# Performance work log

Hardware: AMD Instinct MI355X
Metric: run time of the kernel (lower is better)

## Reference

```python
import jax, jax.numpy as jnp
import numpy as np

N_NODES = 50000
BN_EPS = 1e-5


def sage_conv(x, src, dst, Wl, Wr, b):
    # mean-aggregate neighbor features: message from src -> dst
    msg = x[src]                                             # [E, Din]
    s = jax.ops.segment_sum(msg, dst, num_segments=N_NODES)  # [N, Din]
    cnt = jax.ops.segment_sum(jnp.ones((src.shape[0],), x.dtype), dst,
                              num_segments=N_NODES)          # [N]
    mean = s / jnp.maximum(cnt, 1.0)[:, None]
    # PyG SAGEConv: lin_l(aggregated) (+bias) + lin_r(self), root_weight=True
    return mean @ Wl + b + x @ Wr


def batch_norm(x, gamma, beta):
    mu = jnp.mean(x, axis=0)
    var = jnp.var(x, axis=0)
    return (x - mu) * jax.lax.rsqrt(var + BN_EPS) * gamma + beta


def setup_inputs() -> dict:
    key = jax.random.key(0)
    ks = jax.random.split(key, 16)
    D_IN, D_H, D_OUT = 128, 128, 64
    x = jax.random.normal(ks[0], (N_NODES, D_IN), dtype=jnp.float32)
    edge_index = jax.random.randint(ks[1], (2, 800000), 0, N_NODES, dtype=jnp.int32)

    def xavier(k, din, dout):
        lim = float(np.sqrt(6.0 / (din + dout)))
        return jax.random.uniform(k, (din, dout), jnp.float32, -lim, lim)

    return {
        "x": x, "edge_index": edge_index,
        "Wl0": xavier(ks[2], D_IN, D_H), "Wr0": xavier(ks[3], D_IN, D_H),
        "b0": jnp.zeros((D_H,), jnp.float32),
        "g0": jnp.ones((D_H,), jnp.float32), "be0": jnp.zeros((D_H,), jnp.float32),
        "Wl1": xavier(ks[4], D_H, D_H), "Wr1": xavier(ks[5], D_H, D_H),
        "b1": jnp.zeros((D_H,), jnp.float32),
        "g1": jnp.ones((D_H,), jnp.float32), "be1": jnp.zeros((D_H,), jnp.float32),
        "Wl2": xavier(ks[6], D_H, D_OUT), "Wr2": xavier(ks[7], D_H, D_OUT),
        "b2": jnp.zeros((D_OUT,), jnp.float32),
    }


def reference(x, edge_index, Wl0, Wr0, b0, g0, be0,
              Wl1, Wr1, b1, g1, be1, Wl2, Wr2, b2):
    src, dst = edge_index[0], edge_index[1]
    h = sage_conv(x, src, dst, Wl0, Wr0, b0)
    h = jax.nn.relu(batch_norm(h, g0, be0))
    h = sage_conv(h, src, dst, Wl1, Wr1, b1)
    h = jax.nn.relu(batch_norm(h, g1, be1))
    h = sage_conv(h, src, dst, Wl2, Wr2, b2)
    return jax.nn.log_softmax(h, axis=-1)
```

## Files before the change

kernel.cpp:

```cpp
#include <hip/hip_runtime.h>
#include <hip/hip_bf16.h>

#define D_IN 128
#define D_OUT 64
#define BN_EPS 1e-5f
#define NB_PART 512

typedef short short8 __attribute__((ext_vector_type(8)));
typedef float f32x4 __attribute__((ext_vector_type(4)));
typedef float f32x2 __attribute__((ext_vector_type(2)));
typedef unsigned short ushort_t;
typedef unsigned int uint_t;

__device__ __forceinline__ float bf16lo(uint_t v) { return __uint_as_float(v << 16); }
__device__ __forceinline__ float bf16hi(uint_t v) { return __uint_as_float(v & 0xffff0000u); }
__device__ __forceinline__ ushort_t f2bf(float f) {
    union { __hip_bfloat16 h; ushort_t u; } cv;
    cv.h = __float2bfloat16(f);
    return cv.u;
}
__device__ __forceinline__ f32x4 ntload4(const float* p) {
    return __builtin_nontemporal_load((const f32x4*)p);
}


__global__ void hist_kernel(const int* __restrict__ dst, int* __restrict__ cnt, int E) {
    int i = blockIdx.x * 256 + threadIdx.x;
    if (i < E) atomicAdd(&cnt[__builtin_nontemporal_load(&dst[i])], 1);
}

__global__ void scan_part_kernel(const int* __restrict__ cnt, int* __restrict__ bsum, int n) {
    int i = blockIdx.x * 256 + threadIdx.x;
    int v = (i < n) ? cnt[i] : 0;
#pragma unroll
    for (int off = 1; off < 64; off <<= 1) v += __shfl_xor(v, off);
    __shared__ int ws[4];
    int lane = threadIdx.x & 63, wid = threadIdx.x >> 6;
    if (lane == 0) ws[wid] = v;
    __syncthreads();
    if (threadIdx.x == 0) bsum[blockIdx.x] = ws[0] + ws[1] + ws[2] + ws[3];
}

__global__ void scan_mid_kernel(const int* __restrict__ bsum, int* __restrict__ bpre,
                                int* __restrict__ offs, int PB, int n) {
    int t = threadIdx.x;
    int v = (t < PB) ? bsum[t] : 0;
    int lane = t & 63, wid = t >> 6;
    int sc = v;
#pragma unroll
    for (int off = 1; off < 64; off <<= 1) {
        int u = __shfl_up(sc, off);
        if (lane >= off) sc += u;
    }
    __shared__ int ws[4];
    if (lane == 63) ws[wid] = sc;
    __syncthreads();
    int wb = 0;
    for (int w = 0; w < 4; w++) if (w < wid) wb += ws[w];
    int incl = sc + wb;
    if (t < PB) bpre[t] = incl - v;
    if (t == PB - 1) offs[n] = incl;
}

__global__ void scan_final_kernel(const int* __restrict__ cnt, const int* __restrict__ bpre,
                                  int* __restrict__ offs, int* __restrict__ cursor, int n) {
    int b = blockIdx.x, t = threadIdx.x;
    int i = b * 256 + t;
    int v = (i < n) ? cnt[i] : 0;
    int lane = t & 63, wid = t >> 6;
    int sc = v;
#pragma unroll
    for (int off = 1; off < 64; off <<= 1) {
        int u = __shfl_up(sc, off);
        if (lane >= off) sc += u;
    }
    __shared__ int ws[4];
    if (lane == 63) ws[wid] = sc;
    __syncthreads();
    int wb = 0;
    for (int w = 0; w < 4; w++) if (w < wid) wb += ws[w];
    if (i < n) {
        int e = bpre[b] + wb + sc - v;
        offs[i] = e;
        cursor[i] = e;
    }
}

__global__ void scatter_kernel(const int* __restrict__ src, const int* __restrict__ dst,
                               int* __restrict__ cursor, ushort_t* __restrict__ sorted_src,
                               int E, int passW) {
    int lo = blockIdx.y * passW, hi = lo + passW;
    int i = blockIdx.x * 256 + threadIdx.x;
    if (i < E) {
        int d = __builtin_nontemporal_load(&dst[i]);
        if (d >= lo && d < hi) {
            int s = __builtin_nontemporal_load(&src[i]);
            int p = atomicAdd(&cursor[d], 1);
            sorted_src[p] = (ushort_t)s;
        }
    }
}


__global__ void wswz_kernel(const float* __restrict__ Wl0, const float* __restrict__ Wr0,
                            const float* __restrict__ Wl1, const float* __restrict__ Wr1,
                            const float* __restrict__ Wl2, const float* __restrict__ Wr2,
                            short* __restrict__ o0l, short* __restrict__ o0r,
                            short* __restrict__ o1l, short* __restrict__ o1r,
                            short* __restrict__ o2l, short* __restrict__ o2r) {
    int layer = blockIdx.z;
    int Nn = (layer == 2) ? 64 : 128;
    const float* W;
    short* out;
    if (layer == 0) { W = blockIdx.y ? Wr0 : Wl0; out = blockIdx.y ? o0r : o0l; }
    else if (layer == 1) { W = blockIdx.y ? Wr1 : Wl1; out = blockIdx.y ? o1r : o1l; }
    else { W = blockIdx.y ? Wr2 : Wl2; out = blockIdx.y ? o2r : o2l; }
    int g = blockIdx.x * 256 + threadIdx.x;
    int nchunks = (Nn / 16) * 4;
    int chunk = g >> 6, lane = g & 63;
    if (chunk >= nchunks) return;
    int nf = chunk >> 2, kk = chunk & 3;
    short8 s;
#pragma unroll
    for (int j = 0; j < 8; j++) {
        float v = W[(size_t)(kk * 32 + (lane >> 4) * 8 + j) * Nn + nf * 16 + (lane & 15)];
        s[j] = (short)f2bf(v);
    }
    *(short8*)&out[((size_t)(chunk << 6) + lane) * 8] = s;
}


template <int TN, bool BN>
__global__ __launch_bounds__(TN == 128 ? 256 : 128)
void gemm2_mfma(const float* __restrict__ A, const short* __restrict__ WlF,
                const short* __restrict__ WrF, ushort_t* __restrict__ Yb,
                float* __restrict__ Z, const float* __restrict__ stats,
                const float* __restrict__ gamma, const float* __restrict__ beta, int M) {
    __shared__ short As[64 * 136];
    __shared__ float sc[128], sh[128];
    const int tid = threadIdx.x;
    const int lane = tid & 63;
    const int w = tid >> 6;
    const int row0 = blockIdx.x * 64;
    const int NT = (TN == 128) ? 256 : 128;

    if (BN) {
        if (tid < 128) {
            float invM = 1.0f / (float)M;
            float mu = stats[tid] * invM;
            float var = stats[128 + tid] * invM - mu * mu;
            float scale = gamma[tid] * rsqrtf(var + BN_EPS);
            sc[tid] = scale;
            sh[tid] = beta[tid] - mu * scale;
        }
        __syncthreads();
    }

    for (int c = tid; c < 1024; c += NT) {
        int r = c >> 4, off = (c & 15) * 8;
        short8 v8 = {0, 0, 0, 0, 0, 0, 0, 0};
        if (row0 + r < M) {
            const float* ap = &A[(size_t)(row0 + r) * 128 + off];
            f32x4 f0 = ntload4(ap);
            f32x4 f1 = ntload4(ap + 4);
            if (BN) {
#pragma unroll
                for (int j = 0; j < 4; j++) {
                    f0[j] = fmaxf(f0[j] * sc[off + j] + sh[off + j], 0.f);
                    f1[j] = fmaxf(f1[j] * sc[off + 4 + j] + sh[off + 4 + j], 0.f);
                }
            }
#pragma unroll
            for (int j = 0; j < 4; j++) {
                v8[j] = (short)f2bf(f0[j]);
                v8[4 + j] = (short)f2bf(f1[j]);
            }
        }
        *(short8*)&As[r * 136 + off] = v8;
    }
    __syncthreads();

    const short* WF;
    bool isY;
    int col0;
    if (TN == 128) {
        isY = (w < 2);
        WF = isY ? WlF : WrF;
        col0 = (w & 1) * 64;
    } else {
        isY = (w == 0);
        WF = isY ? WlF : WrF;
        col0 = 0;
    }

    short8 a[4][4];
#pragma unroll
    for (int m = 0; m < 4; m++)
#pragma unroll
        for (int kk = 0; kk < 4; kk++)
            a[m][kk] = *(const short8*)&As[(m * 16 + (lane & 15)) * 136 + kk * 32 + (lane >> 4) * 8];

    f32x4 acc[4][4];
#pragma unroll
    for (int m = 0; m < 4; m++)
#pragma unroll
        for (int n = 0; n < 4; n++) acc[m][n] = (f32x4){0.f, 0.f, 0.f, 0.f};

#pragma unroll
    for (int kk = 0; kk < 4; kk++) {
#pragma unroll
        for (int n = 0; n < 4; n++) {
            short8 b = *(const short8*)&WF[(size_t)(((col0 >> 4) + n) * 4 + kk) * 512 + lane * 8];
#pragma unroll
            for (int m = 0; m < 4; m++)
                acc[m][n] = __builtin_amdgcn_mfma_f32_16x16x32_bf16(a[m][kk], b, acc[m][n], 0, 0, 0);
        }
    }

#pragma unroll
    for (int m = 0; m < 4; m++) {
#pragma unroll
        for (int i = 0; i < 4; i++) {
            int gr = row0 + m * 16 + (lane >> 4) * 4 + i;
            if (gr < M) {
                if (isY) {
#pragma unroll
                    for (int n = 0; n < 4; n++)
                        Yb[(size_t)gr * TN + col0 + n * 16 + (lane & 15)] = f2bf(acc[m][n][i]);
                } else {
#pragma unroll
                    for (int n = 0; n < 4; n++)
                        Z[(size_t)gr * TN + col0 + n * 16 + (lane & 15)] = acc[m][n][i];
                }
            }
        }
    }
}


__global__ __launch_bounds__(256) void agg128_kernel(const ushort_t* __restrict__ Yb,
                                                     const int* __restrict__ offs,
                                                     const ushort_t* __restrict__ sorted_src,
                                                     const float* __restrict__ bias,
                                                     float* __restrict__ H, int N) {
    int node = blockIdx.x * 4 + (threadIdx.x >> 6);
    int lane = threadIdx.x & 63;
    if (node >= N) return;
    int s0 = offs[node], s1 = offs[node + 1];
    float a0 = 0.f, a1 = 0.f;
    int k = s0;
    for (; k + 8 <= s1; k += 8) {
        int idx[8];
#pragma unroll
        for (int j = 0; j < 8; j++) idx[j] = __builtin_nontemporal_load(&sorted_src[k + j]);
        uint_t v[8];
#pragma unroll
        for (int j = 0; j < 8; j++) v[j] = *(const uint_t*)&Yb[(size_t)idx[j] * 128 + lane * 2];
#pragma unroll
        for (int j = 0; j < 8; j++) {
            a0 += bf16lo(v[j]);
            a1 += bf16hi(v[j]);
        }
    }
    if (k + 4 <= s1) {
        int idx[4];
#pragma unroll
        for (int j = 0; j < 4; j++) idx[j] = __builtin_nontemporal_load(&sorted_src[k + j]);
#pragma unroll
        for (int j = 0; j < 4; j++) {
            uint_t v = *(const uint_t*)&Yb[(size_t)idx[j] * 128 + lane * 2];
            a0 += bf16lo(v);
            a1 += bf16hi(v);
        }
        k += 4;
    }
    for (; k < s1; k++) {
        uint_t v = *(const uint_t*)&Yb[(size_t)sorted_src[k] * 128 + lane * 2];
        a0 += bf16lo(v);
        a1 += bf16hi(v);
    }
    float inv = 1.0f / fmaxf((float)(s1 - s0), 1.0f);
    float2 b = *(const float2*)&bias[lane * 2];
    f32x2* hp = (f32x2*)&H[(size_t)node * 128 + lane * 2];
    f32x2 h = __builtin_nontemporal_load(hp);
    h[0] += a0 * inv + b.x;
    h[1] += a1 * inv + b.y;
    __builtin_nontemporal_store(h, hp);
}


__global__ __launch_bounds__(256) void agg_lsm_kernel(const ushort_t* __restrict__ Yb,
                                                      const int* __restrict__ offs,
                                                      const ushort_t* __restrict__ sorted_src,
                                                      const float* __restrict__ bias,
                                                      const float* __restrict__ Z,
                                                      float* __restrict__ out, int N) {
    int wv = blockIdx.x * 4 + (threadIdx.x >> 6);
    int lane = threadIdx.x & 63;
    int half = lane >> 5, l = lane & 31;
    int node = wv * 2 + half;
    if (node >= N) return;
    int s0 = offs[node], s1 = offs[node + 1];
    float a0 = 0.f, a1 = 0.f;
    int k = s0;
    for (; k + 4 <= s1; k += 4) {
        int idx[4];
#pragma unroll
        for (int j = 0; j < 4; j++) idx[j] = __builtin_nontemporal_load(&sorted_src[k + j]);
#pragma unroll
        for (int j = 0; j < 4; j++) {
            uint_t v = *(const uint_t*)&Yb[(size_t)idx[j] * 64 + l * 2];
            a0 += bf16lo(v);
            a1 += bf16hi(v);
        }
    }
    for (; k < s1; k++) {
        uint_t v = *(const uint_t*)&Yb[(size_t)sorted_src[k] * 64 + l * 2];
        a0 += bf16lo(v);
        a1 += bf16hi(v);
    }
    float inv = 1.0f / fmaxf((float)(s1 - s0), 1.0f);
    f32x2 zb = __builtin_nontemporal_load((const f32x2*)&Z[(size_t)node * 64 + l * 2]);
    float2 bb = *(const float2*)&bias[l * 2];
    float v0 = zb[0] + a0 * inv + bb.x;
    float v1 = zb[1] + a1 * inv + bb.y;
    float m = fmaxf(v0, v1);
#pragma unroll
    for (int off = 16; off; off >>= 1) m = fmaxf(m, __shfl_xor(m, off));
    float s = expf(v0 - m) + expf(v1 - m);
#pragma unroll
    for (int off = 16; off; off >>= 1) s += __shfl_xor(s, off);
    float ls = logf(s);
    f32x2 o;
    o[0] = v0 - m - ls;
    o[1] = v1 - m - ls;
    __builtin_nontemporal_store(o, (f32x2*)&out[(size_t)node * 64 + l * 2]);
}


__global__ __launch_bounds__(256) void bn_part_kernel(const float* __restrict__ H,
                                                      float* __restrict__ P, int M) {
    int b = blockIdx.x;
    int R = (M + NB_PART - 1) / NB_PART;
    int r0 = b * R, r1 = min(r0 + R, M);
    int colg = (threadIdx.x & 31) * 4;
    int rowoff = threadIdx.x >> 5;
    f32x4 s = {0.f, 0.f, 0.f, 0.f}, s2 = {0.f, 0.f, 0.f, 0.f};
    for (int r = r0 + rowoff; r < r1; r += 8) {
        f32x4 v = ntload4(&H[(size_t)r * 128 + colg]);
        s += v;
        s2 += v * v;
    }
    __shared__ float ls[256][8];
#pragma unroll
    for (int j = 0; j < 4; j++) {
        ls[threadIdx.x][j] = s[j];
        ls[threadIdx.x][4 + j] = s2[j];
    }
    __syncthreads();
    if (threadIdx.x < 32) {
#pragma unroll
        for (int j = 0; j < 8; j++) {
            float a = 0.f;
#pragma unroll
            for (int k = 0; k < 8; k++) a += ls[threadIdx.x + 32 * k][j];
            if (j < 4) P[(size_t)b * 256 + threadIdx.x * 4 + j] = a;
            else P[(size_t)b * 256 + 128 + threadIdx.x * 4 + (j - 4)] = a;
        }
    }
}

__global__ __launch_bounds__(1024) void bn_reduce_kernel(const float* __restrict__ P,
                                                         float* __restrict__ stats) {
    int c = threadIdx.x & 255, q = threadIdx.x >> 8;
    float acc = 0.f;
#pragma unroll 8
    for (int i = q * (NB_PART / 4); i < (q + 1) * (NB_PART / 4); i++)
        acc += P[(size_t)i * 256 + c];
    __shared__ float ls[4][256];
    ls[q][c] = acc;
    __syncthreads();
    if (threadIdx.x < 256) stats[c] = ls[0][c] + ls[1][c] + ls[2][c] + ls[3][c];
}


extern "C" void kernel_launch(void* const* d_in, const int* in_sizes, int n_in,
                              void* d_out, int out_size, void* d_ws, size_t ws_size,
                              hipStream_t stream) {
    const float* x   = (const float*)d_in[0];
    const int*   ei  = (const int*)d_in[1];
    const float* Wl0 = (const float*)d_in[2];
    const float* Wr0 = (const float*)d_in[3];
    const float* b0  = (const float*)d_in[4];
    const float* g0  = (const float*)d_in[5];
    const float* be0 = (const float*)d_in[6];
    const float* Wl1 = (const float*)d_in[7];
    const float* Wr1 = (const float*)d_in[8];
    const float* b1  = (const float*)d_in[9];
    const float* g1  = (const float*)d_in[10];
    const float* be1 = (const float*)d_in[11];
    const float* Wl2 = (const float*)d_in[12];
    const float* Wr2 = (const float*)d_in[13];
    const float* b2  = (const float*)d_in[14];

    const int N = in_sizes[0] / D_IN;
    const int E = in_sizes[1] / 2;
    const int PB = (N + 255) / 256;

    float* H = (float*)d_ws;
    float* Z2 = H + (size_t)N * D_IN;
    ushort_t* Yb = (ushort_t*)(Z2 + (size_t)N * D_OUT);
    int* cnt    = (int*)(Yb + (size_t)N * D_IN);
    int* offs   = cnt + N;
    int* cursor = offs + N + 1;
    int* bsum   = cursor + N;
    int* bpre   = bsum + 256;
    ushort_t* sorted = (ushort_t*)(bpre + 256);
    float* stats = (float*)(sorted + E + (E & 1));
    float* P = stats + 512;
    short* WlF0 = (short*)(P + NB_PART * 256);
    short* WrF0 = WlF0 + 16384;
    short* WlF1 = WrF0 + 16384;
    short* WrF1 = WlF1 + 16384;
    short* WlF2 = WrF1 + 16384;
    short* WrF2 = WlF2 + 8192;

    const int eb = (E + 255) / 256;

    hipMemsetAsync(cnt, 0, (size_t)N * sizeof(int), stream);
    hist_kernel<<<eb, 256, 0, stream>>>(ei + E, cnt, E);
    scan_part_kernel<<<PB, 256, 0, stream>>>(cnt, bsum, N);
    scan_mid_kernel<<<1, 256, 0, stream>>>(bsum, bpre, offs, PB, N);
    scan_final_kernel<<<PB, 256, 0, stream>>>(cnt, bpre, offs, cursor, N);
    scatter_kernel<<<dim3(eb, 2), 256, 0, stream>>>(ei, ei + E, cursor, sorted, E, (N + 1) / 2);

    wswz_kernel<<<dim3(8, 2, 3), 256, 0, stream>>>(Wl0, Wr0, Wl1, Wr1, Wl2, Wr2,
                                                   WlF0, WrF0, WlF1, WrF1, WlF2, WrF2);

    const int gb = (N + 63) / 64;
    const int ab = (N + 3) / 4;
    const int ab2 = (N + 7) / 8;

    gemm2_mfma<128, false><<<gb, 256, 0, stream>>>(x, WlF0, WrF0, Yb, H,
                                                   nullptr, nullptr, nullptr, N);
    agg128_kernel<<<ab, 256, 0, stream>>>(Yb, offs, sorted, b0, H, N);
    bn_part_kernel<<<NB_PART, 256, 0, stream>>>(H, P, N);
    bn_reduce_kernel<<<1, 1024, 0, stream>>>(P, stats);

    gemm2_mfma<128, true><<<gb, 256, 0, stream>>>(H, WlF1, WrF1, Yb, H,
                                                  stats, g0, be0, N);
    agg128_kernel<<<ab, 256, 0, stream>>>(Yb, offs, sorted, b1, H, N);
    bn_part_kernel<<<NB_PART, 256, 0, stream>>>(H, P, N);
    bn_reduce_kernel<<<1, 1024, 0, stream>>>(P, stats + 256);

    gemm2_mfma<64, true><<<gb, 128, 0, stream>>>(H, WlF2, WrF2, Yb, Z2,
                                                 stats + 256, g1, be1, N);
    agg_lsm_kernel<<<ab2, 256, 0, stream>>>(Yb, offs, sorted, b2, Z2, (float*)d_out, N);
}
```

Before: 372.8 us.

## Store hidden activations and root-term outputs in bf16 instead of fp32

Converts the intermediate H (post-aggregation hidden) and Z (self-term GEMM output) buffers from fp32 to bf16 across the GEMM, aggregation, batch-norm statistics and log-softmax kernels. This roughly halves the memory traffic of the bandwidth-bound intermediate writes and reads. The aggregation kernel is reworked to process two nodes per wavefront with 4 columns per lane, and the BN partial reduction now reads 8 bf16 values per thread. The cost is extra rounding error in the hidden activations and in the BN statistics computed from them.

```diff
diff --git a/kernel.cpp b/kernel.cpp
--- a/kernel.cpp
+++ b/kernel.cpp
@@ -9,11 +9,14 @@
 typedef short short8 __attribute__((ext_vector_type(8)));
 typedef float f32x4 __attribute__((ext_vector_type(4)));
 typedef float f32x2 __attribute__((ext_vector_type(2)));
+typedef unsigned int u32x4 __attribute__((ext_vector_type(4)));
+typedef unsigned int u32x2 __attribute__((ext_vector_type(2)));
 typedef unsigned short ushort_t;
 typedef unsigned int uint_t;
 
 __device__ __forceinline__ float bf16lo(uint_t v) { return __uint_as_float(v << 16); }
 __device__ __forceinline__ float bf16hi(uint_t v) { return __uint_as_float(v & 0xffff0000u); }
+__device__ __forceinline__ float bf2f(ushort_t u) { return __uint_as_float(((uint_t)u) << 16); }
 __device__ __forceinline__ ushort_t f2bf(float f) {
     union { __hip_bfloat16 h; ushort_t u; } cv;
     cv.h = __float2bfloat16(f);
@@ -130,11 +133,11 @@
 }
 
 
-template <int TN, bool BN>
+template <int TN, bool BF16IN>
 __global__ __launch_bounds__(TN == 128 ? 256 : 128)
-void gemm2_mfma(const float* __restrict__ A, const short* __restrict__ WlF,
+void gemm2_mfma(const void* __restrict__ Ain, const short* __restrict__ WlF,
                 const short* __restrict__ WrF, ushort_t* __restrict__ Yb,
-                float* __restrict__ Z, const float* __restrict__ stats,
+                ushort_t* __restrict__ Zb, const float* __restrict__ stats,
                 const float* __restrict__ gamma, const float* __restrict__ beta, int M) {
     __shared__ short As[64 * 136];
     __shared__ float sc[128], sh[128];
@@ -144,7 +147,7 @@
     const int row0 = blockIdx.x * 64;
     const int NT = (TN == 128) ? 256 : 128;
 
-    if (BN) {
+    if (BF16IN) {
         if (tid < 128) {
             float invM = 1.0f / (float)M;
             float mu = stats[tid] * invM;
@@ -160,36 +163,42 @@
         int r = c >> 4, off = (c & 15) * 8;
         short8 v8 = {0, 0, 0, 0, 0, 0, 0, 0};
         if (row0 + r < M) {
-            const float* ap = &A[(size_t)(row0 + r) * 128 + off];
-            f32x4 f0 = ntload4(ap);
-            f32x4 f1 = ntload4(ap + 4);
-            if (BN) {
+            if (BF16IN) {
+                const ushort_t* ap = (const ushort_t*)Ain + (size_t)(row0 + r) * 128 + off;
+                short8 h = *(const short8*)ap;
+#pragma unroll
+                for (int j = 0; j < 8; j++) {
+                    float f = bf2f((ushort_t)h[j]);
+                    f = fmaxf(f * sc[off + j] + sh[off + j], 0.f);
+                    v8[j] = (short)f2bf(f);
+                }
+            } else {
+                const float* ap = (const float*)Ain + (size_t)(row0 + r) * 128 + off;
+                f32x4 f0 = ntload4(ap);
+                f32x4 f1 = ntload4(ap + 4);
 #pragma unroll
                 for (int j = 0; j < 4; j++) {
-                    f0[j] = fmaxf(f0[j] * sc[off + j] + sh[off + j], 0.f);
-                    f1[j] = fmaxf(f1[j] * sc[off + 4 + j] + sh[off + 4 + j], 0.f);
+                    v8[j] = (short)f2bf(f0[j]);
+                    v8[4 + j] = (short)f2bf(f1[j]);
                 }
             }
-#pragma unroll
-            for (int j = 0; j < 4; j++) {
-                v8[j] = (short)f2bf(f0[j]);
-                v8[4 + j] = (short)f2bf(f1[j]);
-            }
         }
         *(short8*)&As[r * 136 + off] = v8;
     }
     __syncthreads();
 
     const short* WF;
-    bool isY;
+    ushort_t* D;
     int col0;
     if (TN == 128) {
-        isY = (w < 2);
+        bool isY = (w < 2);
         WF = isY ? WlF : WrF;
+        D = isY ? Yb : Zb;
         col0 = (w & 1) * 64;
     } else {
-        isY = (w == 0);
+        bool isY = (w == 0);
         WF = isY ? WlF : WrF;
+        D = isY ? Yb : Zb;
         col0 = 0;
     }
 
@@ -223,15 +232,9 @@
         for (int i = 0; i < 4; i++) {
             int gr = row0 + m * 16 + (lane >> 4) * 4 + i;
             if (gr < M) {
-                if (isY) {
-#pragma unroll
-                    for (int n = 0; n < 4; n++)
-                        Yb[(size_t)gr * TN + col0 + n * 16 + (lane & 15)] = f2bf(acc[m][n][i]);
-                } else {
-#pragma unroll
-                    for (int n = 0; n < 4; n++)
-                        Z[(size_t)gr * TN + col0 + n * 16 + (lane & 15)] = acc[m][n][i];
-                }
+#pragma unroll
+                for (int n = 0; n < 4; n++)
+                    D[(size_t)gr * TN + col0 + n * 16 + (lane & 15)] = f2bf(acc[m][n][i]);
             }
         }
     }
@@ -242,24 +245,29 @@
                                                      const int* __restrict__ offs,
                                                      const ushort_t* __restrict__ sorted_src,
                                                      const float* __restrict__ bias,
-                                                     float* __restrict__ H, int N) {
-    int node = blockIdx.x * 4 + (threadIdx.x >> 6);
+                                                     const ushort_t* __restrict__ Zb,
+                                                     ushort_t* __restrict__ Hb, int N) {
+    int wv = blockIdx.x * 4 + (threadIdx.x >> 6);
     int lane = threadIdx.x & 63;
+    int half = lane >> 5, l = lane & 31;
+    int node = wv * 2 + half;
     if (node >= N) return;
     int s0 = offs[node], s1 = offs[node + 1];
-    float a0 = 0.f, a1 = 0.f;
+    float a0 = 0.f, a1 = 0.f, a2 = 0.f, a3 = 0.f;
     int k = s0;
     for (; k + 8 <= s1; k += 8) {
         int idx[8];
 #pragma unroll
         for (int j = 0; j < 8; j++) idx[j] = __builtin_nontemporal_load(&sorted_src[k + j]);
-        uint_t v[8];
-#pragma unroll
-        for (int j = 0; j < 8; j++) v[j] = *(const uint_t*)&Yb[(size_t)idx[j] * 128 + lane * 2];
+        u32x2 v[8];
+#pragma unroll
+        for (int j = 0; j < 8; j++) v[j] = *(const u32x2*)&Yb[(size_t)idx[j] * 128 + l * 4];
 #pragma unroll
         for (int j = 0; j < 8; j++) {
-            a0 += bf16lo(v[j]);
-            a1 += bf16hi(v[j]);
+            a0 += bf16lo(v[j][0]);
+            a1 += bf16hi(v[j][0]);
+            a2 += bf16lo(v[j][1]);
+            a3 += bf16hi(v[j][1]);
         }
     }
     if (k + 4 <= s1) {
@@ -268,24 +276,32 @@
         for (int j = 0; j < 4; j++) idx[j] = __builtin_nontemporal_load(&sorted_src[k + j]);
 #pragma unroll
         for (int j = 0; j < 4; j++) {
-            uint_t v = *(const uint_t*)&Yb[(size_t)idx[j] * 128 + lane * 2];
-            a0 += bf16lo(v);
-            a1 += bf16hi(v);
+            u32x2 v = *(const u32x2*)&Yb[(size_t)idx[j] * 128 + l * 4];
+            a0 += bf16lo(v[0]);
+            a1 += bf16hi(v[0]);
+            a2 += bf16lo(v[1]);
+            a3 += bf16hi(v[1]);
         }
         k += 4;
     }
     for (; k < s1; k++) {
-        uint_t v = *(const uint_t*)&Yb[(size_t)sorted_src[k] * 128 + lane * 2];
-        a0 += bf16lo(v);
-        a1 += bf16hi(v);
+        u32x2 v = *(const u32x2*)&Yb[(size_t)sorted_src[k] * 128 + l * 4];
+        a0 += bf16lo(v[0]);
+        a1 += bf16hi(v[0]);
+        a2 += bf16lo(v[1]);
+        a3 += bf16hi(v[1]);
     }
     float inv = 1.0f / fmaxf((float)(s1 - s0), 1.0f);
-    float2 b = *(const float2*)&bias[lane * 2];
-    f32x2* hp = (f32x2*)&H[(size_t)node * 128 + lane * 2];
-    f32x2 h = __builtin_nontemporal_load(hp);
-    h[0] += a0 * inv + b.x;
-    h[1] += a1 * inv + b.y;
-    __builtin_nontemporal_store(h, hp);
+    float4 bb = *(const float4*)&bias[l * 4];
+    u32x2 z = __builtin_nontemporal_load((const u32x2*)&Zb[(size_t)node * 128 + l * 4]);
+    float h0 = bf16lo(z[0]) + a0 * inv + bb.x;
+    float h1 = bf16hi(z[0]) + a1 * inv + bb.y;
+    float h2 = bf16lo(z[1]) + a2 * inv + bb.z;
+    float h3 = bf16hi(z[1]) + a3 * inv + bb.w;
+    u32x2 o;
+    o[0] = (uint_t)f2bf(h0) | ((uint_t)f2bf(h1) << 16);
+    o[1] = (uint_t)f2bf(h2) | ((uint_t)f2bf(h3) << 16);
+    __builtin_nontemporal_store(o, (u32x2*)&Hb[(size_t)node * 128 + l * 4]);
 }
 
 
@@ -293,7 +309,7 @@
                                                       const int* __restrict__ offs,
                                                       const ushort_t* __restrict__ sorted_src,
                                                       const float* __restrict__ bias,
-                                                      const float* __restrict__ Z,
+                                                      const ushort_t* __restrict__ Zb,
                                                       float* __restrict__ out, int N) {
     int wv = blockIdx.x * 4 + (threadIdx.x >> 6);
     int lane = threadIdx.x & 63;
@@ -320,10 +336,10 @@
         a1 += bf16hi(v);
     }
     float inv = 1.0f / fmaxf((float)(s1 - s0), 1.0f);
-    f32x2 zb = __builtin_nontemporal_load((const f32x2*)&Z[(size_t)node * 64 + l * 2]);
+    uint_t z = *(const uint_t*)&Zb[(size_t)node * 64 + l * 2];
     float2 bb = *(const float2*)&bias[l * 2];
-    float v0 = zb[0] + a0 * inv + bb.x;
-    float v1 = zb[1] + a1 * inv + bb.y;
+    float v0 = bf16lo(z) + a0 * inv + bb.x;
+    float v1 = bf16hi(z) + a1 * inv + bb.y;
     float m = fmaxf(v0, v1);
 #pragma unroll
     for (int off = 16; off; off >>= 1) m = fmaxf(m, __shfl_xor(m, off));
@@ -338,35 +354,46 @@
 }
 
 
-__global__ __launch_bounds__(256) void bn_part_kernel(const float* __restrict__ H,
+__global__ __launch_bounds__(256) void bn_part_kernel(const ushort_t* __restrict__ Hb,
                                                       float* __restrict__ P, int M) {
     int b = blockIdx.x;
     int R = (M + NB_PART - 1) / NB_PART;
     int r0 = b * R, r1 = min(r0 + R, M);
-    int colg = (threadIdx.x & 31) * 4;
-    int rowoff = threadIdx.x >> 5;
-    f32x4 s = {0.f, 0.f, 0.f, 0.f}, s2 = {0.f, 0.f, 0.f, 0.f};
-    for (int r = r0 + rowoff; r < r1; r += 8) {
-        f32x4 v = ntload4(&H[(size_t)r * 128 + colg]);
-        s += v;
-        s2 += v * v;
-    }
-    __shared__ float ls[256][8];
-#pragma unroll
-    for (int j = 0; j < 4; j++) {
+    int colg = (threadIdx.x & 15) * 8;
+    int rowoff = threadIdx.x >> 4;
+    float s[8], s2[8];
+#pragma unroll
+    for (int j = 0; j < 8; j++) { s[j] = 0.f; s2[j] = 0.f; }
+    for (int r = r0 + rowoff; r < r1; r += 16) {
+        u32x4 v = __builtin_nontemporal_load((const u32x4*)&Hb[(size_t)r * 128 + colg]);
+#pragma unroll
+        for (int q = 0; q < 4; q++) {
+            float flo = bf16lo(v[q]);
+            float fhi = bf16hi(v[q]);
+            s[2 * q] += flo;
+            s2[2 * q] += flo * flo;
+            s[2 * q + 1] += fhi;
+            s2[2 * q + 1] += fhi * fhi;
+        }
+    }
+    __shared__ float ls[256][16];
+#pragma unroll
+    for (int j = 0; j < 8; j++) {
         ls[threadIdx.x][j] = s[j];
-        ls[threadIdx.x][4 + j] = s2[j];
-    }
-    __syncthreads();
-    if (threadIdx.x < 32) {
-#pragma unroll
-        for (int j = 0; j < 8; j++) {
-            float a = 0.f;
-#pragma unroll
-            for (int k = 0; k < 8; k++) a += ls[threadIdx.x + 32 * k][j];
-            if (j < 4) P[(size_t)b * 256 + threadIdx.x * 4 + j] = a;
-            else P[(size_t)b * 256 + 128 + threadIdx.x * 4 + (j - 4)] = a;
-        }
+        ls[threadIdx.x][8 + j] = s2[j];
+    }
+    __syncthreads();
+    if (threadIdx.x < 128) {
+        int g = threadIdx.x >> 3, j = threadIdx.x & 7;
+        float a = 0.f, c = 0.f;
+#pragma unroll
+        for (int kk = 0; kk < 16; kk++) {
+            int id = kk * 16 + g;
+            a += ls[id][j];
+            c += ls[id][8 + j];
+        }
+        P[(size_t)b * 256 + threadIdx.x] = a;
+        P[(size_t)b * 256 + 128 + threadIdx.x] = c;
     }
 }
 
@@ -407,9 +434,9 @@
     const int E = in_sizes[1] / 2;
     const int PB = (N + 255) / 256;
 
-    float* H = (float*)d_ws;
-    float* Z2 = H + (size_t)N * D_IN;
-    ushort_t* Yb = (ushort_t*)(Z2 + (size_t)N * D_OUT);
+    ushort_t* Hb = (ushort_t*)d_ws;
+    ushort_t* Zb = Hb + (size_t)N * D_IN;
+    ushort_t* Yb = Zb + (size_t)N * D_IN;
     int* cnt    = (int*)(Yb + (size_t)N * D_IN);
     int* offs   = cnt + N;
     int* cursor = offs + N + 1;
@@ -438,22 +465,21 @@
                                                    WlF0, WrF0, WlF1, WrF1, WlF2, WrF2);
 
     const int gb = (N + 63) / 64;
-    const int ab = (N + 3) / 4;
-    const int ab2 = (N + 7) / 8;
-
-    gemm2_mfma<128, false><<<gb, 256, 0, stream>>>(x, WlF0, WrF0, Yb, H,
+    const int ab = (N + 7) / 8;
+
+    gemm2_mfma<128, false><<<gb, 256, 0, stream>>>(x, WlF0, WrF0, Yb, Zb,
                                                    nullptr, nullptr, nullptr, N);
-    agg128_kernel<<<ab, 256, 0, stream>>>(Yb, offs, sorted, b0, H, N);
-    bn_part_kernel<<<NB_PART, 256, 0, stream>>>(H, P, N);
+    agg128_kernel<<<ab, 256, 0, stream>>>(Yb, offs, sorted, b0, Zb, Hb, N);
+    bn_part_kernel<<<NB_PART, 256, 0, stream>>>(Hb, P, N);
     bn_reduce_kernel<<<1, 1024, 0, stream>>>(P, stats);
 
-    gemm2_mfma<128, true><<<gb, 256, 0, stream>>>(H, WlF1, WrF1, Yb, H,
+    gemm2_mfma<128, true><<<gb, 256, 0, stream>>>(Hb, WlF1, WrF1, Yb, Zb,
                                                   stats, g0, be0, N);
-    agg128_kernel<<<ab, 256, 0, stream>>>(Yb, offs, sorted, b1, H, N);
-    bn_part_kernel<<<NB_PART, 256, 0, stream>>>(H, P, N);
+    agg128_kernel<<<ab, 256, 0, stream>>>(Yb, offs, sorted, b1, Zb, Hb, N);
+    bn_part_kernel<<<NB_PART, 256, 0, stream>>>(Hb, P, N);
     bn_reduce_kernel<<<1, 1024, 0, stream>>>(P, stats + 256);
 
-    gemm2_mfma<64, true><<<gb, 128, 0, stream>>>(H, WlF2, WrF2, Yb, Z2,
+    gemm2_mfma<64, true><<<gb, 128, 0, stream>>>(Hb, WlF2, WrF2, Yb, Zb,
                                                  stats + 256, g1, be1, N);
-    agg_lsm_kernel<<<ab2, 256, 0, stream>>>(Yb, offs, sorted, b2, Z2, (float*)d_out, N);
-}
+    agg_lsm_kernel<<<ab, 256, 0, stream>>>(Yb, offs, sorted, b2, Zb, (float*)d_out, N);
+}
```

After: 347.5 us. 6.8% less time.
